# Kernel optimization log

Hardware: AMD Instinct MI355X
Metric: run time of the kernel (lower is better)

Reference implementation:

```python
import jax, jax.numpy as jnp
import numpy as np

HIDDEN = 1024

def setup_inputs() -> dict:
    key = jax.random.key(0)
    k1, k2, k3, k4, k5 = jax.random.split(key, 5)
    B, T, E2, H = 32, 2048, 1024, HIDDEN
    scale = 1.0 / np.sqrt(H)
    x = jax.random.normal(k1, (B, T, E2), dtype=jnp.float32)
    W_ih = jax.random.uniform(k2, (4 * H, E2), minval=-scale, maxval=scale, dtype=jnp.float32)
    W_hh = jax.random.uniform(k3, (4 * H, H), minval=-scale, maxval=scale, dtype=jnp.float32)
    b_ih = jax.random.uniform(k4, (4 * H,), minval=-scale, maxval=scale, dtype=jnp.float32)
    b_hh = jax.random.uniform(k5, (4 * H,), minval=-scale, maxval=scale, dtype=jnp.float32)
    return {"x": x, "W_ih": W_ih, "W_hh": W_hh, "b_ih": b_ih, "b_hh": b_hh}

def reference(x, W_ih, W_hh, b_ih, b_hh):
    B, T, _ = x.shape
    H = W_hh.shape[1]
    # Precompute input contribution for all timesteps: [T, B, 4H]
    x_proj = jnp.einsum('bte,ge->tbg', x, W_ih) + b_ih + b_hh

    def step(carry, xp_t):
        h, c = carry
        gates = xp_t + h @ W_hh.T  # [B, 4H]
        i, f, g, o = jnp.split(gates, 4, axis=-1)  # torch gate order i,f,g,o
        i = jax.nn.sigmoid(i)
        f = jax.nn.sigmoid(f)
        g = jnp.tanh(g)
        o = jax.nn.sigmoid(o)
        c_new = f * c + i * g
        h_new = o * jnp.tanh(c_new)
        return (h_new, c_new), None

    h0 = jnp.zeros((B, H), dtype=x.dtype)
    c0 = jnp.zeros((B, H), dtype=x.dtype)
    (h_t, c_t), _ = jax.lax.scan(step, (h0, c0), x_proj)
    return (h_t, c_t)
```

## Files before the change

### kernel.cpp

```cpp
#include <hip/hip_runtime.h>
#include <stdint.h>

#define T_STEPS 2048
#define HID 1024
#define G4 4096
#define NWG 64

typedef __attribute__((ext_vector_type(8))) short short8;
typedef __attribute__((ext_vector_type(4))) float float4v;
typedef unsigned long long ull;

#define HBUF_OFF 0ull
#define FLAG_OFF 131072ull
#define DT_OFF   131584ull
#define CST_OFF  135168ull
#define XP_OFF   0x100000ull

__device__ inline unsigned short f2bf(float f) {
  union { float f; unsigned int u; } v; v.f = f;
  unsigned int u = v.u;
  return (unsigned short)((u + 0x7fffu + ((u >> 16) & 1u)) >> 16);
}
__device__ inline float bf2f(unsigned short h) {
  union { unsigned int u; float f; } v; v.u = ((unsigned int)h) << 16;
  return v.f;
}
__device__ inline short8 pack8(float4 a, float4 b) {
  short8 r;
  r[0] = (short)f2bf(a.x); r[1] = (short)f2bf(a.y);
  r[2] = (short)f2bf(a.z); r[3] = (short)f2bf(a.w);
  r[4] = (short)f2bf(b.x); r[5] = (short)f2bf(b.y);
  r[6] = (short)f2bf(b.z); r[7] = (short)f2bf(b.w);
  return r;
}

__global__ void dtype_sniff(const unsigned short* __restrict__ w,
                            unsigned int* __restrict__ dt) {
  __shared__ int red[256];
  const int tid = threadIdx.x;
  int cnt = 0;
#pragma unroll
  for (int i = 0; i < 4; i++) {
    unsigned short h = w[tid * 4 + i];
    unsigned e = (h >> 7) & 0xFF;
    if (h == 0 || (e >= 100 && e <= 123)) cnt++;
  }
  red[tid] = cnt;
  __syncthreads();
  for (int s = 128; s > 0; s >>= 1) {
    if (tid < s) red[tid] += red[tid + s];
    __syncthreads();
  }
  if (tid == 0) dt[0] = (red[0] >= 922) ? 1u : 0u;
}

__global__ __launch_bounds__(256) void xproj_gemm(
    const void* __restrict__ x, const void* __restrict__ Wih,
    const void* __restrict__ bih, const void* __restrict__ bhh,
    unsigned short* __restrict__ xp, int t0,
    const unsigned int* __restrict__ dt)
{
  __shared__ char smem[32768];
  __shared__ float bias_s[128];
  unsigned short* As = (unsigned short*)smem;
  unsigned short* Bs = (unsigned short*)(smem + 10240);

  const bool isbf = (*dt != 0);

  const int bid = blockIdx.x;
  const int panel = bid >> 9;
  const int within = bid & 511;
  const int nt = within & 31;
  const int mt = (panel << 4) + (within >> 5);
  const int m0 = mt * 128;
  const int n0 = nt * 128;
  const int tl0 = m0 >> 5;

  const int tid = threadIdx.x;
  if (tid < 128) {
    bias_s[tid] = isbf
        ? bf2f(((const unsigned short*)bih)[n0 + tid]) +
          bf2f(((const unsigned short*)bhh)[n0 + tid])
        : ((const float*)bih)[n0 + tid] + ((const float*)bhh)[n0 + tid];
  }

  const int w = tid >> 6, lane = tid & 63;
  const int quad = lane >> 4, lr = lane & 15;
  const int wm = (w & 1) * 64, wn = (w >> 1) * 64;

  float4v acc[4][4];
#pragma unroll
  for (int i = 0; i < 4; i++)
#pragma unroll
    for (int j = 0; j < 4; j++) acc[i][j] = (float4v){0.f, 0.f, 0.f, 0.f};

  const int r = tid >> 1, half = tid & 1;
  const size_t aoff =
      ((size_t)(r & 31) * T_STEPS + (size_t)(t0 + tl0 + (r >> 5))) * HID + half * 16;
  const size_t boff = (size_t)(n0 + r) * HID + half * 16;
  unsigned short* adst = As + r * 40 + half * 16;
  unsigned short* bdst = Bs + r * 40 + half * 16;

  for (int k0 = 0; k0 < HID; k0 += 32) {
    __syncthreads();
    if (isbf) {
      const unsigned short* a16 = (const unsigned short*)x + aoff + k0;
      const unsigned short* b16 = (const unsigned short*)Wih + boff + k0;
      *(short8*)(adst)     = *(const short8*)(a16);
      *(short8*)(adst + 8) = *(const short8*)(a16 + 8);
      *(short8*)(bdst)     = *(const short8*)(b16);
      *(short8*)(bdst + 8) = *(const short8*)(b16 + 8);
    } else {
      const float4* af = (const float4*)((const float*)x + aoff + k0);
      const float4* bf = (const float4*)((const float*)Wih + boff + k0);
      float4 a0 = af[0], a1 = af[1], a2 = af[2], a3 = af[3];
      float4 b0 = bf[0], b1 = bf[1], b2 = bf[2], b3 = bf[3];
      *(short8*)(adst)     = pack8(a0, a1);
      *(short8*)(adst + 8) = pack8(a2, a3);
      *(short8*)(bdst)     = pack8(b0, b1);
      *(short8*)(bdst + 8) = pack8(b2, b3);
    }
    __syncthreads();
    short8 afr[4], bfr[4];
#pragma unroll
    for (int i = 0; i < 4; i++)
      afr[i] = *(const short8*)(As + (wm + i * 16 + lr) * 40 + quad * 8);
#pragma unroll
    for (int j = 0; j < 4; j++)
      bfr[j] = *(const short8*)(Bs + (wn + j * 16 + lr) * 40 + quad * 8);
#pragma unroll
    for (int i = 0; i < 4; i++)
#pragma unroll
      for (int j = 0; j < 4; j++)
        acc[i][j] = __builtin_amdgcn_mfma_f32_16x16x32_bf16(afr[i], bfr[j], acc[i][j], 0, 0, 0);
  }

  __syncthreads();
  unsigned short* ep = (unsigned short*)smem;
#pragma unroll
  for (int i = 0; i < 4; i++)
#pragma unroll
    for (int j = 0; j < 4; j++)
#pragma unroll
      for (int rr = 0; rr < 4; rr++) {
        int ml = wm + i * 16 + quad * 4 + rr;
        int nl = wn + j * 16 + lr;
        float v = acc[i][j][rr] + bias_s[nl];
        ep[(((ml >> 5) * 128) + nl) * 32 + (ml & 31)] = f2bf(v);
      }
  __syncthreads();
#pragma unroll
  for (int tl = 0; tl < 4; tl++) {
    const uint4* s4 = (const uint4*)(smem + tl * 8192);
    uint4* d4 = (uint4*)(xp + ((size_t)(tl0 + tl) * G4 + n0) * 32);
    for (int i = tid; i < 512; i += 256) d4[i] = s4[i];
  }
}

__global__ __launch_bounds__(256, 1) void lstm_rec(
    const void* __restrict__ Whh,
    const unsigned short* __restrict__ xp,
    unsigned short* __restrict__ hbuf,
    unsigned int* __restrict__ flags,
    float* __restrict__ cstate,
    void* __restrict__ out,
    int t0, int tc,
    const unsigned int* __restrict__ dt)
{
  __shared__ __align__(16) unsigned short hs[32 * 1032];
  __shared__ float gbuf[64][33];
  __shared__ __align__(8) unsigned short hout[32][16];

  const bool isbf = (*dt != 0);
  const int wg = blockIdx.x;
  const int tid = threadIdx.x;
  const int w = tid >> 6, lane = tid & 63;
  const int quad = lane >> 4, lr = lane & 15;

  short8 bfrag[32];
  {
    const size_t grow = (size_t)w * HID + wg * 16 + lr;
    if (isbf) {
      const unsigned short* wrow = (const unsigned short*)Whh + grow * HID;
#pragma unroll
      for (int s = 0; s < 32; s++)
        bfrag[s] = *(const short8*)(wrow + s * 32 + quad * 8);
    } else {
      const float* wrow = (const float*)Whh + grow * HID;
#pragma unroll
      for (int s = 0; s < 32; s++) {
        float4 f0 = *(const float4*)(wrow + s * 32 + quad * 8);
        float4 f1 = *(const float4*)(wrow + s * 32 + quad * 8 + 4);
        bfrag[s] = pack8(f0, f1);
      }
    }
  }

  const int eb = tid & 31;
  const int ej = tid >> 5;
  const int gc0 = wg * 16 + ej;
  const int gc1 = gc0 + 8;
  float cs0 = cstate[(size_t)eb * HID + gc0];
  float cs1 = cstate[(size_t)eb * HID + gc1];
  long budget = 50000000;

  for (int t = t0; t < t0 + tc; t++) {
    const unsigned short* xpt = xp + (size_t)(t - t0) * (G4 * 32);
    unsigned short rx0 = xpt[(size_t)gc0 * 32 + eb];
    unsigned short rx1 = xpt[(size_t)(HID + gc0) * 32 + eb];
    unsigned short rx2 = xpt[(size_t)(2 * HID + gc0) * 32 + eb];
    unsigned short rx3 = xpt[(size_t)(3 * HID + gc0) * 32 + eb];
    unsigned short rx4 = xpt[(size_t)gc1 * 32 + eb];
    unsigned short rx5 = xpt[(size_t)(HID + gc1) * 32 + eb];
    unsigned short rx6 = xpt[(size_t)(2 * HID + gc1) * 32 + eb];
    unsigned short rx7 = xpt[(size_t)(3 * HID + gc1) * 32 + eb];

    if (tid >= 64 && tid < 128) {
      while (__hip_atomic_load(&flags[tid - 64], __ATOMIC_RELAXED,
                               __HIP_MEMORY_SCOPE_AGENT) < (unsigned)t) {
        if (--budget < 0) break;
        __builtin_amdgcn_s_sleep(1);
      }
    }
    __syncthreads();

    {
      const ull* src = (const ull*)hbuf + (size_t)(t & 1) * 8192;
      ull v[32];
#pragma unroll
      for (int i = 0; i < 32; i++)
        v[i] = __hip_atomic_load(src + i * 256 + tid, __ATOMIC_RELAXED,
                                 __HIP_MEMORY_SCOPE_AGENT);
#pragma unroll
      for (int i = 0; i < 32; i++) {
        const int idx = i * 256 + tid;
        const int wgp = idx >> 7;
        const int q   = idx & 127;
        const int row = q >> 2, c4 = q & 3;
        *(ull*)((char*)hs + row * 2064 + wgp * 32 + c4 * 8) = v[i];
      }
    }
    __syncthreads();

    float4v acc00 = (float4v){0.f, 0.f, 0.f, 0.f};
    float4v acc01 = (float4v){0.f, 0.f, 0.f, 0.f};
    float4v acc10 = (float4v){0.f, 0.f, 0.f, 0.f};
    float4v acc11 = (float4v){0.f, 0.f, 0.f, 0.f};
    {
      const unsigned short* ar0 = hs + (size_t)lr * 1032 + quad * 8;
      const unsigned short* ar1 = hs + (size_t)(16 + lr) * 1032 + quad * 8;
#pragma unroll
      for (int s = 0; s < 32; s += 2) {
        short8 a00 = *(const short8*)(ar0 + s * 32);
        short8 a01 = *(const short8*)(ar0 + s * 32 + 32);
        short8 a10 = *(const short8*)(ar1 + s * 32);
        short8 a11 = *(const short8*)(ar1 + s * 32 + 32);
        acc00 = __builtin_amdgcn_mfma_f32_16x16x32_bf16(a00, bfrag[s],     acc00, 0, 0, 0);
        acc01 = __builtin_amdgcn_mfma_f32_16x16x32_bf16(a01, bfrag[s + 1], acc01, 0, 0, 0);
        acc10 = __builtin_amdgcn_mfma_f32_16x16x32_bf16(a10, bfrag[s],     acc10, 0, 0, 0);
        acc11 = __builtin_amdgcn_mfma_f32_16x16x32_bf16(a11, bfrag[s + 1], acc11, 0, 0, 0);
      }
    }
    {
      float4v g0 = acc00 + acc01;
      float4v g1 = acc10 + acc11;
      const int lc = w * 16 + lr;
#pragma unroll
      for (int rr = 0; rr < 4; rr++) {
        gbuf[lc][quad * 4 + rr]      = g0[rr];
        gbuf[lc][16 + quad * 4 + rr] = g1[rr];
      }
    }
    __syncthreads();

    {
      float gi0 = gbuf[ej][eb]      + bf2f(rx0);
      float gf0 = gbuf[16 + ej][eb] + bf2f(rx1);
      float gg0 = gbuf[32 + ej][eb] + bf2f(rx2);
      float go0 = gbuf[48 + ej][eb] + bf2f(rx3);
      float si0 = 1.f / (1.f + __expf(-gi0));
      float sf0 = 1.f / (1.f + __expf(-gf0));
      float tg0 = tanhf(gg0);
      float so0 = 1.f / (1.f + __expf(-go0));
      cs0 = sf0 * cs0 + si0 * tg0;
      float hn0 = so0 * tanhf(cs0);
      hout[eb][ej] = f2bf(hn0);

      float gi1 = gbuf[8 + ej][eb]  + bf2f(rx4);
      float gf1 = gbuf[24 + ej][eb] + bf2f(rx5);
      float gg1 = gbuf[40 + ej][eb] + bf2f(rx6);
      float go1 = gbuf[56 + ej][eb] + bf2f(rx7);
      float si1 = 1.f / (1.f + __expf(-gi1));
      float sf1 = 1.f / (1.f + __expf(-gf1));
      float tg1 = tanhf(gg1);
      float so1 = 1.f / (1.f + __expf(-go1));
      cs1 = sf1 * cs1 + si1 * tg1;
      float hn1 = so1 * tanhf(cs1);
      hout[eb][8 + ej] = f2bf(hn1);

      if (t == T_STEPS - 1) {
        if (isbf) {
          unsigned short* ob = (unsigned short*)out;
          ob[(size_t)eb * HID + gc0] = f2bf(hn0);
          ob[(size_t)eb * HID + gc1] = f2bf(hn1);
          ob[32768 + (size_t)eb * HID + gc0] = f2bf(cs0);
          ob[32768 + (size_t)eb * HID + gc1] = f2bf(cs1);
        } else {
          float* of = (float*)out;
          of[(size_t)eb * HID + gc0] = hn0;
          of[(size_t)eb * HID + gc1] = hn1;
          of[32768 + (size_t)eb * HID + gc0] = cs0;
          of[32768 + (size_t)eb * HID + gc1] = cs1;
        }
      }
    }
    __syncthreads();

    if (w == 0) {
      const int row = lane >> 1, half = lane & 1;
      ull* dst = (ull*)hbuf + (size_t)((t + 1) & 1) * 8192 +
                 (size_t)wg * 128 + row * 4 + half * 2;
      const ull* hv = (const ull*)&hout[row][half * 8];
      ull h0 = hv[0], h1 = hv[1];
      __hip_atomic_store(dst,     h0, __ATOMIC_RELAXED, __HIP_MEMORY_SCOPE_AGENT);
      __hip_atomic_store(dst + 1, h1, __ATOMIC_RELAXED, __HIP_MEMORY_SCOPE_AGENT);
      asm volatile("s_waitcnt vmcnt(0)" ::: "memory");
      if (lane == 0)
        __hip_atomic_store(&flags[wg], (unsigned)(t + 1), __ATOMIC_RELAXED,
                           __HIP_MEMORY_SCOPE_AGENT);
    }
  }

  cstate[(size_t)eb * HID + gc0] = cs0;
  cstate[(size_t)eb * HID + gc1] = cs1;
}

extern "C" void kernel_launch(void* const* d_in, const int* in_sizes, int n_in,
                              void* d_out, int out_size, void* d_ws, size_t ws_size,
                              hipStream_t stream) {
  (void)in_sizes; (void)n_in; (void)out_size;
  const void* x   = d_in[0];
  const void* Wih = d_in[1];
  const void* Whh = d_in[2];
  const void* bih = d_in[3];
  const void* bhh = d_in[4];

  char* ws = (char*)d_ws;
  unsigned short* hbuf   = (unsigned short*)(ws + HBUF_OFF);
  unsigned int*   flags  = (unsigned int*)(ws + FLAG_OFF);
  unsigned int*   dt     = (unsigned int*)(ws + DT_OFF);
  float*          cstate = (float*)(ws + CST_OFF);
  unsigned short* xp     = (unsigned short*)(ws + XP_OFF);

  int tc = 2048;
  while (tc > 16 && XP_OFF + (size_t)tc * 262144ull > ws_size) tc >>= 1;

  hipMemsetAsync(ws, 0, CST_OFF + 131072, stream);

  hipLaunchKernelGGL(dtype_sniff, dim3(1), dim3(256), 0, stream,
                     (const unsigned short*)Wih, dt);

  for (int t0 = 0; t0 < T_STEPS; t0 += tc) {
    hipLaunchKernelGGL(xproj_gemm, dim3(tc * 8), dim3(256), 0, stream,
                       x, Wih, bih, bhh, xp, t0, dt);
    hipLaunchKernelGGL(lstm_rec, dim3(NWG), dim3(256), 0, stream,
                       Whh, xp, hbuf, flags, cstate, d_out, t0, tc, dt);
  }
}
```

Baseline: 12.91 ms.

## Per-wave flags, direct h stores in MFMA layout, drop hout staging and barriers

Each wave now writes its bf16 h outputs straight to the global h buffer in a layout matching the MFMA A-operand order and sets its own per-wave flag. This removes the hout staging buffer, one __syncthreads, and the single-wave publish step. All waves poll 256 flags cooperatively, replacing the dedicated poller wave and its barrier. The h buffer is read with sc0 sc1 dwordx4 loads and copied to LDS without rearrangement. The cost is more flags to poll, every wave spinning, and possible LDS bank conflicts from the unpadded layout.

```diff
diff --git a/kernel.cpp b/kernel.cpp
--- a/kernel.cpp
+++ b/kernel.cpp
@@ -8,11 +8,12 @@
 
 typedef __attribute__((ext_vector_type(8))) short short8;
 typedef __attribute__((ext_vector_type(4))) float float4v;
+typedef __attribute__((ext_vector_type(4))) unsigned int uint4v;
 typedef unsigned long long ull;
 
 #define HBUF_OFF 0ull
 #define FLAG_OFF 131072ull
-#define DT_OFF   131584ull
+#define DT_OFF   132608ull
 #define CST_OFF  135168ull
 #define XP_OFF   0x100000ull
 
@@ -167,9 +168,8 @@
     int t0, int tc,
     const unsigned int* __restrict__ dt)
 {
-  __shared__ __align__(16) unsigned short hs[32 * 1032];
+  __shared__ __align__(16) unsigned short hs[32768];
   __shared__ float gbuf[64][33];
-  __shared__ __align__(8) unsigned short hout[32][16];
 
   const bool isbf = (*dt != 0);
   const int wg = blockIdx.x;
@@ -196,49 +196,58 @@
     }
   }
 
-  const int eb = tid & 31;
-  const int ej = tid >> 5;
-  const int gc0 = wg * 16 + ej;
-  const int gc1 = gc0 + 8;
-  float cs0 = cstate[(size_t)eb * HID + gc0];
-  float cs1 = cstate[(size_t)eb * HID + gc1];
+  const int b  = 8 * w + (lane >> 3);
+  const int k8 = lane & 7;
+  const int j0 = 2 * k8, j1 = j0 + 1;
+  const int gc0 = wg * 16 + j0, gc1 = gc0 + 1;
+  float cs0 = cstate[(size_t)b * HID + gc0];
+  float cs1 = cstate[(size_t)b * HID + gc1];
   long budget = 50000000;
 
   for (int t = t0; t < t0 + tc; t++) {
     const unsigned short* xpt = xp + (size_t)(t - t0) * (G4 * 32);
-    unsigned short rx0 = xpt[(size_t)gc0 * 32 + eb];
-    unsigned short rx1 = xpt[(size_t)(HID + gc0) * 32 + eb];
-    unsigned short rx2 = xpt[(size_t)(2 * HID + gc0) * 32 + eb];
-    unsigned short rx3 = xpt[(size_t)(3 * HID + gc0) * 32 + eb];
-    unsigned short rx4 = xpt[(size_t)gc1 * 32 + eb];
-    unsigned short rx5 = xpt[(size_t)(HID + gc1) * 32 + eb];
-    unsigned short rx6 = xpt[(size_t)(2 * HID + gc1) * 32 + eb];
-    unsigned short rx7 = xpt[(size_t)(3 * HID + gc1) * 32 + eb];
-
-    if (tid >= 64 && tid < 128) {
-      while (__hip_atomic_load(&flags[tid - 64], __ATOMIC_RELAXED,
-                               __HIP_MEMORY_SCOPE_AGENT) < (unsigned)t) {
+    unsigned short rx0 = xpt[(size_t)gc0 * 32 + b];
+    unsigned short rx1 = xpt[(size_t)(HID + gc0) * 32 + b];
+    unsigned short rx2 = xpt[(size_t)(2 * HID + gc0) * 32 + b];
+    unsigned short rx3 = xpt[(size_t)(3 * HID + gc0) * 32 + b];
+    unsigned short rx4 = xpt[(size_t)gc1 * 32 + b];
+    unsigned short rx5 = xpt[(size_t)(HID + gc1) * 32 + b];
+    unsigned short rx6 = xpt[(size_t)(2 * HID + gc1) * 32 + b];
+    unsigned short rx7 = xpt[(size_t)(3 * HID + gc1) * 32 + b];
+
+    {
+      const unsigned target = (unsigned)t;
+      const unsigned int* fp = flags + 4 * lane;
+      for (;;) {
+        unsigned f0 = __hip_atomic_load(fp + 0, __ATOMIC_RELAXED, __HIP_MEMORY_SCOPE_AGENT);
+        unsigned f1 = __hip_atomic_load(fp + 1, __ATOMIC_RELAXED, __HIP_MEMORY_SCOPE_AGENT);
+        unsigned f2 = __hip_atomic_load(fp + 2, __ATOMIC_RELAXED, __HIP_MEMORY_SCOPE_AGENT);
+        unsigned f3 = __hip_atomic_load(fp + 3, __ATOMIC_RELAXED, __HIP_MEMORY_SCOPE_AGENT);
+        unsigned m01 = f0 < f1 ? f0 : f1;
+        unsigned m23 = f2 < f3 ? f2 : f3;
+        unsigned mn  = m01 < m23 ? m01 : m23;
+        if (mn >= target) break;
         if (--budget < 0) break;
-        __builtin_amdgcn_s_sleep(1);
-      }
-    }
-    __syncthreads();
-
-    {
-      const ull* src = (const ull*)hbuf + (size_t)(t & 1) * 8192;
-      ull v[32];
-#pragma unroll
-      for (int i = 0; i < 32; i++)
-        v[i] = __hip_atomic_load(src + i * 256 + tid, __ATOMIC_RELAXED,
-                                 __HIP_MEMORY_SCOPE_AGENT);
-#pragma unroll
-      for (int i = 0; i < 32; i++) {
-        const int idx = i * 256 + tid;
-        const int wgp = idx >> 7;
-        const int q   = idx & 127;
-        const int row = q >> 2, c4 = q & 3;
-        *(ull*)((char*)hs + row * 2064 + wgp * 32 + c4 * 8) = v[i];
-      }
+      }
+    }
+
+    {
+      const uint4v* src = (const uint4v*)(hbuf + (size_t)(t & 1) * 32768) + tid;
+      uint4v v0, v1, v2, v3, v4, v5, v6, v7, v8, v9, v10, v11, v12, v13, v14, v15;
+#define GL(i, dst) \
+      asm volatile("global_load_dwordx4 %0, %1, off sc0 sc1" \
+                   : "=v"(dst) : "v"(src + (i) * 256) : "memory")
+      GL(0, v0);  GL(1, v1);  GL(2, v2);  GL(3, v3);
+      GL(4, v4);  GL(5, v5);  GL(6, v6);  GL(7, v7);
+      GL(8, v8);  GL(9, v9);  GL(10, v10); GL(11, v11);
+      GL(12, v12); GL(13, v13); GL(14, v14); GL(15, v15);
+#undef GL
+      asm volatile("s_waitcnt vmcnt(0)" ::: "memory");
+      uint4v* d = (uint4v*)hs + tid;
+      d[0 * 256]  = v0;  d[1 * 256]  = v1;  d[2 * 256]  = v2;  d[3 * 256]  = v3;
+      d[4 * 256]  = v4;  d[5 * 256]  = v5;  d[6 * 256]  = v6;  d[7 * 256]  = v7;
+      d[8 * 256]  = v8;  d[9 * 256]  = v9;  d[10 * 256] = v10; d[11 * 256] = v11;
+      d[12 * 256] = v12; d[13 * 256] = v13; d[14 * 256] = v14; d[15 * 256] = v15;
     }
     __syncthreads();
 
@@ -247,18 +256,18 @@
     float4v acc10 = (float4v){0.f, 0.f, 0.f, 0.f};
     float4v acc11 = (float4v){0.f, 0.f, 0.f, 0.f};
     {
-      const unsigned short* ar0 = hs + (size_t)lr * 1032 + quad * 8;
-      const unsigned short* ar1 = hs + (size_t)(16 + lr) * 1032 + quad * 8;
+      const char* a0 = (const char*)hs + lr * 64 + quad * 16;
+      const char* a1 = a0 + 1024;
 #pragma unroll
       for (int s = 0; s < 32; s += 2) {
-        short8 a00 = *(const short8*)(ar0 + s * 32);
-        short8 a01 = *(const short8*)(ar0 + s * 32 + 32);
-        short8 a10 = *(const short8*)(ar1 + s * 32);
-        short8 a11 = *(const short8*)(ar1 + s * 32 + 32);
-        acc00 = __builtin_amdgcn_mfma_f32_16x16x32_bf16(a00, bfrag[s],     acc00, 0, 0, 0);
-        acc01 = __builtin_amdgcn_mfma_f32_16x16x32_bf16(a01, bfrag[s + 1], acc01, 0, 0, 0);
-        acc10 = __builtin_amdgcn_mfma_f32_16x16x32_bf16(a10, bfrag[s],     acc10, 0, 0, 0);
-        acc11 = __builtin_amdgcn_mfma_f32_16x16x32_bf16(a11, bfrag[s + 1], acc11, 0, 0, 0);
+        short8 x00 = *(const short8*)(a0 + (size_t)s * 2048);
+        short8 x01 = *(const short8*)(a0 + (size_t)s * 2048 + 2048);
+        short8 x10 = *(const short8*)(a1 + (size_t)s * 2048);
+        short8 x11 = *(const short8*)(a1 + (size_t)s * 2048 + 2048);
+        acc00 = __builtin_amdgcn_mfma_f32_16x16x32_bf16(x00, bfrag[s],     acc00, 0, 0, 0);
+        acc01 = __builtin_amdgcn_mfma_f32_16x16x32_bf16(x01, bfrag[s + 1], acc01, 0, 0, 0);
+        acc10 = __builtin_amdgcn_mfma_f32_16x16x32_bf16(x10, bfrag[s],     acc10, 0, 0, 0);
+        acc11 = __builtin_amdgcn_mfma_f32_16x16x32_bf16(x11, bfrag[s + 1], acc11, 0, 0, 0);
       }
     }
     {
@@ -274,65 +283,58 @@
     __syncthreads();
 
     {
-      float gi0 = gbuf[ej][eb]      + bf2f(rx0);
-      float gf0 = gbuf[16 + ej][eb] + bf2f(rx1);
-      float gg0 = gbuf[32 + ej][eb] + bf2f(rx2);
-      float go0 = gbuf[48 + ej][eb] + bf2f(rx3);
+      float gi0 = gbuf[j0][b]      + bf2f(rx0);
+      float gf0 = gbuf[16 + j0][b] + bf2f(rx1);
+      float gg0 = gbuf[32 + j0][b] + bf2f(rx2);
+      float go0 = gbuf[48 + j0][b] + bf2f(rx3);
       float si0 = 1.f / (1.f + __expf(-gi0));
       float sf0 = 1.f / (1.f + __expf(-gf0));
       float tg0 = tanhf(gg0);
       float so0 = 1.f / (1.f + __expf(-go0));
       cs0 = sf0 * cs0 + si0 * tg0;
       float hn0 = so0 * tanhf(cs0);
-      hout[eb][ej] = f2bf(hn0);
-
-      float gi1 = gbuf[8 + ej][eb]  + bf2f(rx4);
-      float gf1 = gbuf[24 + ej][eb] + bf2f(rx5);
-      float gg1 = gbuf[40 + ej][eb] + bf2f(rx6);
-      float go1 = gbuf[56 + ej][eb] + bf2f(rx7);
+
+      float gi1 = gbuf[j1][b]      + bf2f(rx4);
+      float gf1 = gbuf[16 + j1][b] + bf2f(rx5);
+      float gg1 = gbuf[32 + j1][b] + bf2f(rx6);
+      float go1 = gbuf[48 + j1][b] + bf2f(rx7);
       float si1 = 1.f / (1.f + __expf(-gi1));
       float sf1 = 1.f / (1.f + __expf(-gf1));
       float tg1 = tanhf(gg1);
       float so1 = 1.f / (1.f + __expf(-go1));
       cs1 = sf1 * cs1 + si1 * tg1;
       float hn1 = so1 * tanhf(cs1);
-      hout[eb][8 + ej] = f2bf(hn1);
+
+      unsigned pk = (unsigned)f2bf(hn0) | ((unsigned)f2bf(hn1) << 16);
+      unsigned int* hb32 = (unsigned int*)hbuf;
+      const unsigned idx = (unsigned)(((t + 1) & 1) * 16384 +
+                                      (wg >> 1) * 512 + b * 16 + (wg & 1) * 8 + k8);
+      __hip_atomic_store(hb32 + idx, pk, __ATOMIC_RELAXED, __HIP_MEMORY_SCOPE_AGENT);
 
       if (t == T_STEPS - 1) {
         if (isbf) {
           unsigned short* ob = (unsigned short*)out;
-          ob[(size_t)eb * HID + gc0] = f2bf(hn0);
-          ob[(size_t)eb * HID + gc1] = f2bf(hn1);
-          ob[32768 + (size_t)eb * HID + gc0] = f2bf(cs0);
-          ob[32768 + (size_t)eb * HID + gc1] = f2bf(cs1);
+          ob[(size_t)b * HID + gc0] = f2bf(hn0);
+          ob[(size_t)b * HID + gc1] = f2bf(hn1);
+          ob[32768 + (size_t)b * HID + gc0] = f2bf(cs0);
+          ob[32768 + (size_t)b * HID + gc1] = f2bf(cs1);
         } else {
           float* of = (float*)out;
-          of[(size_t)eb * HID + gc0] = hn0;
-          of[(size_t)eb * HID + gc1] = hn1;
-          of[32768 + (size_t)eb * HID + gc0] = cs0;
-          of[32768 + (size_t)eb * HID + gc1] = cs1;
+          of[(size_t)b * HID + gc0] = hn0;
+          of[(size_t)b * HID + gc1] = hn1;
+          of[32768 + (size_t)b * HID + gc0] = cs0;
+          of[32768 + (size_t)b * HID + gc1] = cs1;
         }
       }
     }
-    __syncthreads();
-
-    if (w == 0) {
-      const int row = lane >> 1, half = lane & 1;
-      ull* dst = (ull*)hbuf + (size_t)((t + 1) & 1) * 8192 +
-                 (size_t)wg * 128 + row * 4 + half * 2;
-      const ull* hv = (const ull*)&hout[row][half * 8];
-      ull h0 = hv[0], h1 = hv[1];
-      __hip_atomic_store(dst,     h0, __ATOMIC_RELAXED, __HIP_MEMORY_SCOPE_AGENT);
-      __hip_atomic_store(dst + 1, h1, __ATOMIC_RELAXED, __HIP_MEMORY_SCOPE_AGENT);
-      asm volatile("s_waitcnt vmcnt(0)" ::: "memory");
-      if (lane == 0)
-        __hip_atomic_store(&flags[wg], (unsigned)(t + 1), __ATOMIC_RELAXED,
-                           __HIP_MEMORY_SCOPE_AGENT);
-    }
-  }
-
-  cstate[(size_t)eb * HID + gc0] = cs0;
-  cstate[(size_t)eb * HID + gc1] = cs1;
+    asm volatile("s_waitcnt vmcnt(0)" ::: "memory");
+    if (lane == 0)
+      __hip_atomic_store(&flags[wg * 4 + w], (unsigned)(t + 1), __ATOMIC_RELAXED,
+                         __HIP_MEMORY_SCOPE_AGENT);
+  }
+
+  cstate[(size_t)b * HID + gc0] = cs0;
+  cstate[(size_t)b * HID + gc1] = cs1;
 }
 
 extern "C" void kernel_launch(void* const* d_in, const int* in_sizes, int n_in,
```

Result: slower. 14.08 ms (+9.0%).
